# Performance work log

Hardware: AMD Instinct MI355X
Metric: run time of the kernel (lower is better)

The kernel has to match this reference:

```python
import jax, jax.numpy as jnp
import numpy as np

# dims: H heads, D=word_size (d_model), E=embed_dim per head, N=seq_len=n, K=linformer k
H, D, E, N, K = 16, 1024, 64, 4096, 256


def setup_inputs() -> dict:
    key = jax.random.key(0)
    ks = jax.random.split(key, 9)
    s = 0.02  # init scale for weights
    return {
        "x":  jax.random.normal(ks[0], (N, D), jnp.float32),
        # per-head QKV linears: torch Linear weight is (out=E, in=D), bias (E,)
        "Wq": jax.random.normal(ks[1], (H, E, D), jnp.float32) * s,
        "bq": jnp.zeros((H, E), jnp.float32),
        "Wk": jax.random.normal(ks[2], (H, E, D), jnp.float32) * s,
        "bk": jnp.zeros((H, E), jnp.float32),
        "Wv": jax.random.normal(ks[3], (H, E, D), jnp.float32) * s,
        "bv": jnp.zeros((H, E), jnp.float32),
        # per-head E/F sequence projections: Linear(n=N, k=K) -> weight (K, N), bias (K,)
        "Ew": jax.random.normal(ks[4], (H, K, N), jnp.float32) * s,
        "Eb": jnp.zeros((H, K), jnp.float32),
        "Fw": jax.random.normal(ks[5], (H, K, N), jnp.float32) * s,
        "Fb": jnp.zeros((H, K), jnp.float32),
        # output projection: Linear(H*E, E, bias=False) -> weight (E, H*E)
        "Wo": jax.random.normal(ks[6], (E, H * E), jnp.float32) * s,
    }


def reference(x, Wq, bq, Wk, bk, Wv, bv, Ew, Eb, Fw, Fb, Wo):
    # per-head Q/K/V projections, batched over heads: (H, N, E)
    q = jnp.einsum('nd,hed->hne', x, Wq) + bq[:, None, :]
    k = jnp.einsum('nd,hed->hne', x, Wk) + bk[:, None, :]
    v = jnp.einsum('nd,hed->hne', x, Wv) + bv[:, None, :]
    # low-rank sequence-length projection of K and V: (H, K, E)
    kp = jnp.einsum('hjn,hne->hje', Ew, k) + Eb[:, :, None]
    vp = jnp.einsum('hjn,hne->hje', Fw, v) + Fb[:, :, None]
    # scaled dot-product attention against projected keys: (H, N, K)
    score = jnp.einsum('hne,hje->hnj', q, kp) / jnp.sqrt(jnp.float32(E))
    attn = jax.nn.softmax(score, axis=-1)
    z = jnp.einsum('hnj,hje->hne', attn, vp)  # (H, N, E)
    # concat heads along feature dim (matches torch.cat(dim=1)): (N, H*E)
    zs = jnp.transpose(z, (1, 0, 2)).reshape(N, H * E)
    # final projection Linear(H*E, E, bias=False)
    return zs @ Wo.T  # (N, E)
```

## Files before the change

### kernel.cpp

```cpp
#include <hip/hip_runtime.h>
#include <hip/hip_bf16.h>

typedef __attribute__((ext_vector_type(4))) float f32x4;
typedef __attribute__((ext_vector_type(8))) short s16x8;
typedef __attribute__((ext_vector_type(4))) short s16x4;
typedef unsigned short u16;


__device__ __forceinline__ f32x4 mfma16(s16x8 a, s16x8 b, f32x4 c) {
    return __builtin_amdgcn_mfma_f32_16x16x32_bf16(a, b, c, 0, 0, 0);
}

__device__ __forceinline__ u16 bf(float f) {
    union { float f; unsigned u; } x; x.f = f;
    return (u16)((x.u + 0x7fffu + ((x.u >> 16) & 1u)) >> 16);
}
__device__ __forceinline__ unsigned pkbf(float a, float b) {
    union { float f; unsigned u; } x, y; x.f = a; y.f = b;
    unsigned ra = x.u + 0x7fffu + ((x.u >> 16) & 1u);
    unsigned rb = y.u + 0x7fffu + ((y.u >> 16) & 1u);
    return (ra >> 16) | (rb & 0xffff0000u);
}
__device__ __forceinline__ s16x8 cvt8(f32x4 lo, f32x4 hi) {
    union { s16x8 v; unsigned u[4]; } r;
    r.u[0] = pkbf(lo.x, lo.y);
    r.u[1] = pkbf(lo.z, lo.w);
    r.u[2] = pkbf(hi.x, hi.y);
    r.u[3] = pkbf(hi.z, hi.w);
    return r.v;
}

__device__ __forceinline__ void gl_lds16(const u16* g, u16* l) {
    __builtin_amdgcn_global_load_lds(
        (const __attribute__((address_space(1))) unsigned*)g,
        (__attribute__((address_space(3))) unsigned*)l, 16, 0, 0);
}


__global__ __launch_bounds__(256) void cvt_kernel(const float* __restrict__ src,
                                                  u16* __restrict__ dst, int n4) {
    int i = blockIdx.x * 256 + threadIdx.x;
    if (i < n4) {
        f32x4 v = ((const f32x4*)src)[i];
        union { s16x4 v; unsigned u[2]; } r;
        r.u[0] = pkbf(v.x, v.y);
        r.u[1] = pkbf(v.z, v.w);
        ((s16x4*)dst)[i] = r.v;
    }
}


__global__ __launch_bounds__(256, 2) void qkv_kernel(
        const u16* __restrict__ xb, const u16* __restrict__ wb,
        const float* __restrict__ bq, const float* __restrict__ bk,
        const float* __restrict__ bv,
        u16* __restrict__ qo, u16* __restrict__ kTo, u16* __restrict__ vTo) {
    __shared__ u16 As[128 * 32];
    __shared__ u16 Bs[128 * 32];
    int bx   = blockIdx.x % 24;
    int by   = blockIdx.x / 24;
    int tid  = threadIdx.x;
    int lane = tid & 63, w = tid >> 6;
    int l15  = lane & 15, quad = lane >> 4;
    int wr   = w >> 1, wc = w & 1;

    const u16* Ag = xb + (size_t)(by * 128 + (tid >> 2)) * 1024 + (tid & 3) * 8;
    const u16* Bg = wb + (size_t)(bx * 128 + (tid >> 2)) * 1024 + (tid & 3) * 8;
    u16* Al = As + tid * 8;
    u16* Bl = Bs + tid * 8;

    const u16* abase = As + (wr * 64 + l15) * 32 + quad * 8;
    const u16* bbase = Bs + (wc * 64 + l15) * 32 + quad * 8;

    f32x4 acc[4][4] = {};
    for (int k0 = 0; k0 < 1024; k0 += 32) {
        gl_lds16(Ag + k0, Al);
        gl_lds16(Ag + 64 * 1024 + k0, Al + 64 * 32);
        gl_lds16(Bg + k0, Bl);
        gl_lds16(Bg + 64 * 1024 + k0, Bl + 64 * 32);
        __syncthreads();
        s16x8 a[4], b[4];
#pragma unroll
        for (int mi = 0; mi < 4; mi++) a[mi] = *(const s16x8*)(abase + mi * 16 * 32);
#pragma unroll
        for (int nj = 0; nj < 4; nj++) b[nj] = *(const s16x8*)(bbase + nj * 16 * 32);
#pragma unroll
        for (int mi = 0; mi < 4; mi++)
#pragma unroll
            for (int nj = 0; nj < 4; nj++) acc[mi][nj] = mfma16(a[mi], b[nj], acc[mi][nj]);
        __syncthreads();
    }

    int fblk = (bx * 128 + wc * 64) >> 6;
    int mat  = fblk >> 4, h = fblk & 15;
    const float* bias = (mat == 0) ? bq : (mat == 1 ? bk : bv);
#pragma unroll
    for (int nj = 0; nj < 4; nj++) {
        int e = nj * 16 + l15;
        float bb = bias[h * 64 + e];
#pragma unroll
        for (int mi = 0; mi < 4; mi++) {
            int n0 = by * 128 + wr * 64 + mi * 16 + quad * 4;
            f32x4 c = acc[mi][nj];
            if (mat == 0) {
                u16* p = qo + ((size_t)h * 4096 + n0) * 64 + e;
#pragma unroll
                for (int r = 0; r < 4; r++) p[(size_t)r * 64] = bf(c[r] + bb);
            } else {
                u16* p = (mat == 1 ? kTo : vTo) + ((size_t)h * 64 + e) * 4096 + n0;
                union { s16x4 v; u16 s[4]; } pk;
#pragma unroll
                for (int r = 0; r < 4; r++) pk.s[r] = bf(c[r] + bb);
                *(s16x4*)p = pk.v;
            }
        }
    }
}


__global__ __launch_bounds__(256, 4) void kpvp_kernel(
        const float* __restrict__ Ew, const float* __restrict__ Fw,
        const u16* __restrict__ kT, const u16* __restrict__ vT,
        float* __restrict__ accb) {
    __shared__ u16 As[128 * 32];
    __shared__ u16 Bs[64 * 32];
    int b    = blockIdx.x;
    int ks   = b & 15, jt = (b >> 4) & 1, h = (b >> 5) & 15, p = b >> 9;
    int tid  = threadIdx.x;
    int lane = tid & 63, w = tid >> 6;
    int l15  = lane & 15, quad = lane >> 4;

    const float* Ab = (p ? Fw : Ew) + ((size_t)h * 256 + jt * 128) * 4096 + ks * 256;
    const u16*  Bb = (p ? vT : kT) + (size_t)h * 64 * 4096 + ks * 256;

    int arow = tid >> 3, acol = (tid & 7) * 4;
    const float* Ag = Ab + (size_t)arow * 4096 + acol;
    u16* Aw = As + arow * 32 + acol;
    const u16* Bg = Bb + (size_t)(tid >> 2) * 4096 + (tid & 3) * 8;
    u16* Bl = Bs + tid * 8;

    const u16* abase = As + (w * 32 + l15) * 32 + quad * 8;
    const u16* bbase = Bs + l15 * 32 + quad * 8;

    f32x4 acc[2][4] = {};
    for (int s = 0; s < 8; s++) {
        int kk = s * 32;
        gl_lds16(Bg + kk, Bl);
#pragma unroll
        for (int ps = 0; ps < 4; ps++) {
            f32x4 v = *(const f32x4*)(Ag + (size_t)ps * 32 * 4096 + kk);
            union { s16x4 q; unsigned u[2]; } r;
            r.u[0] = pkbf(v.x, v.y);
            r.u[1] = pkbf(v.z, v.w);
            *(s16x4*)(Aw + ps * 32 * 32) = r.q;
        }
        __syncthreads();
        s16x8 a[2], bb[4];
#pragma unroll
        for (int mi = 0; mi < 2; mi++) a[mi] = *(const s16x8*)(abase + mi * 16 * 32);
#pragma unroll
        for (int nj = 0; nj < 4; nj++) bb[nj] = *(const s16x8*)(bbase + nj * 16 * 32);
#pragma unroll
        for (int mi = 0; mi < 2; mi++)
#pragma unroll
            for (int nj = 0; nj < 4; nj++) acc[mi][nj] = mfma16(a[mi], bb[nj], acc[mi][nj]);
        __syncthreads();
    }

    float* out = accb + ((size_t)(p * 16 + h) * 256 + jt * 128 + w * 32 + quad * 4) * 64;
#pragma unroll
    for (int mi = 0; mi < 2; mi++)
#pragma unroll
        for (int nj = 0; nj < 4; nj++) {
            int e = nj * 16 + l15;
#pragma unroll
            for (int r = 0; r < 4; r++)
                atomicAdd(out + (size_t)(mi * 16 + r) * 64 + e, acc[mi][nj][r]);
        }
}


__global__ __launch_bounds__(256) void packkv_kernel(
        const float* __restrict__ accb, const float* __restrict__ Eb,
        const float* __restrict__ Fb, u16* __restrict__ kp, u16* __restrict__ vpT) {
    int idx = blockIdx.x * 256 + threadIdx.x;
    int p = idx >> 18, h = (idx >> 14) & 15, j = (idx >> 6) & 255, e = idx & 63;
    float v = accb[idx];
    if (p == 0) {
        v += Eb[h * 256 + j];
        kp[((size_t)(h * 256 + j)) * 64 + e] = bf(v * 0.125f);
    } else {
        v += Fb[h * 256 + j];
        vpT[((size_t)(h * 64 + e)) * 256 + j] = bf(v);
    }
}


__global__ __launch_bounds__(256) void attn_kernel(
        const u16* __restrict__ q, const u16* __restrict__ kp,
        const u16* __restrict__ vpT, u16* __restrict__ zs) {
    __shared__ u16 ps[4][16][256];
    int bm   = blockIdx.x & 63, h = blockIdx.x >> 6;
    int lane = threadIdx.x & 63, w = threadIdx.x >> 6;
    int l15  = lane & 15, quad = lane >> 4;
    int nbase = bm * 64 + w * 16;

    f32x4 s[16] = {};
    const u16* qp  = q  + ((size_t)h * 4096 + nbase + l15) * 64 + quad * 8;
    const u16* kpp = kp + ((size_t)h * 256 + l15) * 64 + quad * 8;
#pragma unroll
    for (int e0 = 0; e0 < 64; e0 += 32) {
        s16x8 a = *(const s16x8*)(qp + e0);
#pragma unroll
        for (int jt = 0; jt < 16; jt++) {
            s16x8 b = *(const s16x8*)(kpp + jt * 16 * 64 + e0);
            s[jt] = mfma16(a, b, s[jt]);
        }
    }

    float lsum[4];
#pragma unroll
    for (int r = 0; r < 4; r++) {
        float m = s[0][r];
#pragma unroll
        for (int jt = 1; jt < 16; jt++) m = fmaxf(m, s[jt][r]);
        m = fmaxf(m, __shfl_xor(m, 1));
        m = fmaxf(m, __shfl_xor(m, 2));
        m = fmaxf(m, __shfl_xor(m, 4));
        m = fmaxf(m, __shfl_xor(m, 8));
        float l = 0.f;
#pragma unroll
        for (int jt = 0; jt < 16; jt++) {
            float pv = __expf(s[jt][r] - m);
            s[jt][r] = pv;
            l += pv;
        }
        l += __shfl_xor(l, 1);
        l += __shfl_xor(l, 2);
        l += __shfl_xor(l, 4);
        l += __shfl_xor(l, 8);
        lsum[r] = l;
    }

#pragma unroll
    for (int jt = 0; jt < 16; jt++)
#pragma unroll
        for (int r = 0; r < 4; r++)
            ps[w][quad * 4 + r][jt * 16 + l15] = bf(s[jt][r]);
    __syncthreads();

    f32x4 z[4] = {};
    const u16* vp = vpT + ((size_t)h * 64 + l15) * 256 + quad * 8;
#pragma unroll
    for (int kj = 0; kj < 8; kj++) {
        s16x8 a = *(const s16x8*)&ps[w][l15][kj * 32 + quad * 8];
#pragma unroll
        for (int et = 0; et < 4; et++) {
            s16x8 b = *(const s16x8*)(vp + et * 16 * 256 + kj * 32);
            z[et] = mfma16(a, b, z[et]);
        }
    }
#pragma unroll
    for (int et = 0; et < 4; et++) {
        int e = et * 16 + l15;
        u16* o = zs + ((size_t)(nbase + quad * 4)) * 1024 + h * 64 + e;
#pragma unroll
        for (int r = 0; r < 4; r++) o[(size_t)r * 1024] = bf(z[et][r] / lsum[r]);
    }
}


__global__ __launch_bounds__(256) void out_kernel(
        const u16* __restrict__ zs, const u16* __restrict__ wob,
        float* __restrict__ out) {
    int ks   = blockIdx.x & 3;
    int bm   = blockIdx.x >> 2;
    int lane = threadIdx.x & 63, w = threadIdx.x >> 6;
    int l15  = lane & 15, quad = lane >> 4;
    int row0 = bm * 128 + w * 32;

    const u16* A = zs  + (size_t)(row0 + l15) * 1024 + ks * 256 + quad * 8;
    const u16* B = wob + (size_t)l15 * 1024 + ks * 256 + quad * 8;

    f32x4 acc[2][4] = {};
    for (int k = 0; k < 256; k += 32) {
        s16x8 a0 = *(const s16x8*)(A + k);
        s16x8 a1 = *(const s16x8*)(A + 16 * 1024 + k);
#pragma unroll
        for (int nt = 0; nt < 4; nt++) {
            s16x8 bv = *(const s16x8*)(B + (size_t)nt * 16 * 1024 + k);
            acc[0][nt] = mfma16(a0, bv, acc[0][nt]);
            acc[1][nt] = mfma16(a1, bv, acc[1][nt]);
        }
    }
#pragma unroll
    for (int mt = 0; mt < 2; mt++)
#pragma unroll
        for (int nt = 0; nt < 4; nt++) {
            int e = nt * 16 + l15;
            int n0 = row0 + mt * 16 + quad * 4;
            float* o = out + (size_t)n0 * 64 + e;
#pragma unroll
            for (int r = 0; r < 4; r++) atomicAdd(o + (size_t)r * 64, acc[mt][nt][r]);
        }
}


extern "C" void kernel_launch(void* const* d_in, const int* in_sizes, int n_in,
                              void* d_out, int out_size, void* d_ws, size_t ws_size,
                              hipStream_t stream) {
    const float* x  = (const float*)d_in[0];
    const float* Wq = (const float*)d_in[1];
    const float* bq = (const float*)d_in[2];
    const float* Wk = (const float*)d_in[3];
    const float* bk = (const float*)d_in[4];
    const float* Wv = (const float*)d_in[5];
    const float* bv = (const float*)d_in[6];
    const float* Ew = (const float*)d_in[7];
    const float* Eb = (const float*)d_in[8];
    const float* Fw = (const float*)d_in[9];
    const float* Fb = (const float*)d_in[10];
    const float* Wo = (const float*)d_in[11];

    char* ws = (char*)d_ws;
    u16*   qb   = (u16*)(ws + 0);
    u16*   kT   = (u16*)(ws + 8388608);
    u16*   vT   = (u16*)(ws + 16777216);
    u16*   zsb  = (u16*)(ws + 25165824);
    float* accb = (float*)(ws + 33554432);
    u16*   kp   = (u16*)(ws + 35651584);
    u16*   vpT  = (u16*)(ws + 36175872);
    u16*   xb   = (u16*)(ws + 36700160);
    u16*   wb   = (u16*)(ws + 45088768);
    u16*   wob  = (u16*)(ws + 51380224);

    hipMemsetAsync(accb, 0, (size_t)2 * 16 * 256 * 64 * sizeof(float), stream);
    hipMemsetAsync(d_out, 0, (size_t)4096 * 64 * sizeof(float), stream);

    cvt_kernel<<<4096, 256, 0, stream>>>(x,  xb, 1048576);
    cvt_kernel<<<1024, 256, 0, stream>>>(Wq, wb,           262144);
    cvt_kernel<<<1024, 256, 0, stream>>>(Wk, wb + 1048576, 262144);
    cvt_kernel<<<1024, 256, 0, stream>>>(Wv, wb + 2097152, 262144);
    cvt_kernel<<<64,   256, 0, stream>>>(Wo, wob, 16384);

    qkv_kernel<<<768, 256, 0, stream>>>(xb, wb, bq, bk, bv, qb, kT, vT);
    kpvp_kernel<<<1024, 256, 0, stream>>>(Ew, Fw, kT, vT, accb);
    packkv_kernel<<<2048, 256, 0, stream>>>(accb, Eb, Fb, kp, vpT);
    attn_kernel<<<1024, 256, 0, stream>>>(qb, kp, vpT, zsb);
    out_kernel<<<128, 256, 0, stream>>>(zsb, wob, (float*)d_out);
}
```

Before: 319.8 us.

## Replace kpvp atomic split-K reduction with per-split partial buffers

The kpvp kernel now writes its split-K partial sums to a separate slice per K-split instead of issuing float atomicAdds into one accumulator. The packkv kernel then sums the 16 slices before adding bias. This removes the memset of the accumulator and the atomic contention. The kpvp kernel also changes its warp tiling to 64x32 per wave and pads the A shared-memory tile to 40 columns to avoid bank conflicts. The qkv kernel occupancy hint rises from 2 to 3 blocks per CU. In exchange, the workspace grows by about 32 MB and packkv reads 16 times as much data.

```diff
diff --git a/kernel.cpp b/kernel.cpp
--- a/kernel.cpp
+++ b/kernel.cpp
@@ -50,7 +50,7 @@
 }
 
 
-__global__ __launch_bounds__(256, 2) void qkv_kernel(
+__global__ __launch_bounds__(256, 3) void qkv_kernel(
         const u16* __restrict__ xb, const u16* __restrict__ wb,
         const float* __restrict__ bq, const float* __restrict__ bk,
         const float* __restrict__ bv,
@@ -121,71 +121,73 @@
 __global__ __launch_bounds__(256, 4) void kpvp_kernel(
         const float* __restrict__ Ew, const float* __restrict__ Fw,
         const u16* __restrict__ kT, const u16* __restrict__ vT,
-        float* __restrict__ accb) {
-    __shared__ u16 As[128 * 32];
+        float* __restrict__ accs) {
+    __shared__ u16 As[128 * 40];
     __shared__ u16 Bs[64 * 32];
     int b    = blockIdx.x;
     int ks   = b & 15, jt = (b >> 4) & 1, h = (b >> 5) & 15, p = b >> 9;
     int tid  = threadIdx.x;
     int lane = tid & 63, w = tid >> 6;
     int l15  = lane & 15, quad = lane >> 4;
-
-    const float* Ab = (p ? Fw : Ew) + ((size_t)h * 256 + jt * 128) * 4096 + ks * 256;
-    const u16*  Bb = (p ? vT : kT) + (size_t)h * 64 * 4096 + ks * 256;
-
-    int arow = tid >> 3, acol = (tid & 7) * 4;
-    const float* Ag = Ab + (size_t)arow * 4096 + acol;
-    u16* Aw = As + arow * 32 + acol;
-    const u16* Bg = Bb + (size_t)(tid >> 2) * 4096 + (tid & 3) * 8;
+    int wm   = w & 1, wn = w >> 1;
+
+    const float* Ag = (p ? Fw : Ew)
+        + (size_t)(h * 256 + jt * 128 + (tid >> 3)) * 4096 + ks * 256 + (tid & 7) * 4;
+    const u16* Bg = (p ? vT : kT)
+        + ((size_t)h * 64 + (tid >> 2)) * 4096 + ks * 256 + (tid & 3) * 8;
+    u16* Aw = As + (tid >> 3) * 40 + (tid & 7) * 4;
     u16* Bl = Bs + tid * 8;
 
-    const u16* abase = As + (w * 32 + l15) * 32 + quad * 8;
-    const u16* bbase = Bs + l15 * 32 + quad * 8;
-
-    f32x4 acc[2][4] = {};
+    const u16* abase = As + (wm * 64 + l15) * 40 + quad * 8;
+    const u16* bbase = Bs + (wn * 32 + l15) * 32 + quad * 8;
+
+    f32x4 acc[4][2] = {};
     for (int s = 0; s < 8; s++) {
         int kk = s * 32;
         gl_lds16(Bg + kk, Bl);
 #pragma unroll
-        for (int ps = 0; ps < 4; ps++) {
-            f32x4 v = *(const f32x4*)(Ag + (size_t)ps * 32 * 4096 + kk);
-            union { s16x4 q; unsigned u[2]; } r;
-            r.u[0] = pkbf(v.x, v.y);
-            r.u[1] = pkbf(v.z, v.w);
-            *(s16x4*)(Aw + ps * 32 * 32) = r.q;
+        for (int pr = 0; pr < 4; pr++) {
+            f32x4 v = *(const f32x4*)(Ag + (size_t)pr * 32 * 4096 + kk);
+            union { s16x4 q; unsigned u[2]; } rr;
+            rr.u[0] = pkbf(v.x, v.y);
+            rr.u[1] = pkbf(v.z, v.w);
+            *(s16x4*)(Aw + pr * 32 * 40) = rr.q;
         }
         __syncthreads();
-        s16x8 a[2], bb[4];
-#pragma unroll
-        for (int mi = 0; mi < 2; mi++) a[mi] = *(const s16x8*)(abase + mi * 16 * 32);
-#pragma unroll
-        for (int nj = 0; nj < 4; nj++) bb[nj] = *(const s16x8*)(bbase + nj * 16 * 32);
-#pragma unroll
-        for (int mi = 0; mi < 2; mi++)
-#pragma unroll
-            for (int nj = 0; nj < 4; nj++) acc[mi][nj] = mfma16(a[mi], bb[nj], acc[mi][nj]);
+        s16x8 a[4], bb2[2];
+#pragma unroll
+        for (int mt = 0; mt < 4; mt++) a[mt] = *(const s16x8*)(abase + mt * 16 * 40);
+#pragma unroll
+        for (int nt = 0; nt < 2; nt++) bb2[nt] = *(const s16x8*)(bbase + nt * 16 * 32);
+#pragma unroll
+        for (int mt = 0; mt < 4; mt++)
+#pragma unroll
+            for (int nt = 0; nt < 2; nt++)
+                acc[mt][nt] = mfma16(a[mt], bb2[nt], acc[mt][nt]);
         __syncthreads();
     }
 
-    float* out = accb + ((size_t)(p * 16 + h) * 256 + jt * 128 + w * 32 + quad * 4) * 64;
-#pragma unroll
-    for (int mi = 0; mi < 2; mi++)
-#pragma unroll
-        for (int nj = 0; nj < 4; nj++) {
-            int e = nj * 16 + l15;
+    size_t base = (size_t)ks * 524288
+        + ((size_t)(p * 16 + h) * 256 + jt * 128 + wm * 64 + quad * 4) * 64
+        + wn * 32 + l15;
+#pragma unroll
+    for (int mt = 0; mt < 4; mt++)
+#pragma unroll
+        for (int nt = 0; nt < 2; nt++)
 #pragma unroll
             for (int r = 0; r < 4; r++)
-                atomicAdd(out + (size_t)(mi * 16 + r) * 64 + e, acc[mi][nj][r]);
-        }
+                accs[base + (size_t)(mt * 16 + r) * 64 + nt * 16] = acc[mt][nt][r];
 }
 
 
 __global__ __launch_bounds__(256) void packkv_kernel(
-        const float* __restrict__ accb, const float* __restrict__ Eb,
+        const float* __restrict__ accs, const float* __restrict__ Eb,
         const float* __restrict__ Fb, u16* __restrict__ kp, u16* __restrict__ vpT) {
     int idx = blockIdx.x * 256 + threadIdx.x;
+    float v = 0.f;
+#pragma unroll
+    for (int s = 0; s < 16; s++) v += accs[idx + (size_t)s * 524288];
     int p = idx >> 18, h = (idx >> 14) & 15, j = (idx >> 6) & 255, e = idx & 63;
-    float v = accb[idx];
     if (p == 0) {
         v += Eb[h * 256 + j];
         kp[((size_t)(h * 256 + j)) * 64 + e] = bf(v * 0.125f);
@@ -327,14 +329,13 @@
     u16*   kT   = (u16*)(ws + 8388608);
     u16*   vT   = (u16*)(ws + 16777216);
     u16*   zsb  = (u16*)(ws + 25165824);
-    float* accb = (float*)(ws + 33554432);
-    u16*   kp   = (u16*)(ws + 35651584);
-    u16*   vpT  = (u16*)(ws + 36175872);
-    u16*   xb   = (u16*)(ws + 36700160);
-    u16*   wb   = (u16*)(ws + 45088768);
-    u16*   wob  = (u16*)(ws + 51380224);
-
-    hipMemsetAsync(accb, 0, (size_t)2 * 16 * 256 * 64 * sizeof(float), stream);
+    float* accs = (float*)(ws + 33554432);
+    u16*   kp   = (u16*)(ws + 67108864);
+    u16*   vpT  = (u16*)(ws + 67633152);
+    u16*   xb   = (u16*)(ws + 68157440);
+    u16*   wb   = (u16*)(ws + 76546048);
+    u16*   wob  = (u16*)(ws + 82837504);
+
     hipMemsetAsync(d_out, 0, (size_t)4096 * 64 * sizeof(float), stream);
 
     cvt_kernel<<<4096, 256, 0, stream>>>(x,  xb, 1048576);
@@ -344,8 +345,8 @@
     cvt_kernel<<<64,   256, 0, stream>>>(Wo, wob, 16384);
 
     qkv_kernel<<<768, 256, 0, stream>>>(xb, wb, bq, bk, bv, qb, kT, vT);
-    kpvp_kernel<<<1024, 256, 0, stream>>>(Ew, Fw, kT, vT, accb);
-    packkv_kernel<<<2048, 256, 0, stream>>>(accb, Eb, Fb, kp, vpT);
+    kpvp_kernel<<<1024, 256, 0, stream>>>(Ew, Fw, kT, vT, accs);
+    packkv_kernel<<<2048, 256, 0, stream>>>(accs, Eb, Fb, kp, vpT);
     attn_kernel<<<1024, 256, 0, stream>>>(qb, kp, vpT, zsb);
     out_kernel<<<128, 256, 0, stream>>>(zsb, wob, (float*)d_out);
 }
```

New measurement: 311.3 us. 2.6% less time.
